# Kernel optimization log

Measured on AMD Instinct MI355X. Metric: run time of the kernel, lower is better.

Reference implementation:

```python
import jax, jax.numpy as jnp
import numpy as np

N_NODES = 100000
N_EDGES = 1600000
F_IN = 128      # dataset.num_features
HID = 128       # hidden_dim (heads=1)
HID_POST = 128  # hidden_dim_post
EDGE_DIM = 16
N_CLASSES = 16
NEG_SLOPE = 0.2  # PyG GATConv default leaky_relu slope


def setup_inputs() -> dict:
    key = jax.random.key(0)
    ks = jax.random.split(key, 16)
    s = 0.1  # weight scale
    inp = {
        "x": jax.random.normal(ks[0], (N_NODES, F_IN), jnp.float32),
        "edge_attr": jax.random.normal(ks[1], (N_EDGES, EDGE_DIM), jnp.float32),
        "W0": jax.random.normal(ks[2], (F_IN, HID), jnp.float32) * s,
        "a_src0": jax.random.normal(ks[3], (HID,), jnp.float32) * s,
        "a_dst0": jax.random.normal(ks[4], (HID,), jnp.float32) * s,
        "We0": jax.random.normal(ks[5], (EDGE_DIM, HID), jnp.float32) * s,
        "a_e0": jax.random.normal(ks[6], (HID,), jnp.float32) * s,
        "b0": jnp.zeros((HID,), jnp.float32),
        "W1": jax.random.normal(ks[7], (HID, HID), jnp.float32) * s,
        "a_src1": jax.random.normal(ks[8], (HID,), jnp.float32) * s,
        "a_dst1": jax.random.normal(ks[9], (HID,), jnp.float32) * s,
        "We1": jax.random.normal(ks[10], (EDGE_DIM, HID), jnp.float32) * s,
        "a_e1": jax.random.normal(ks[11], (HID,), jnp.float32) * s,
        "b1": jnp.zeros((HID,), jnp.float32),
        "lin1_w": jax.random.normal(ks[12], (HID, HID_POST), jnp.float32) * s,
        "lin1_b": jnp.zeros((HID_POST,), jnp.float32),
        "lin2_w": jax.random.normal(ks[13], (HID_POST, N_CLASSES), jnp.float32) * s,
        "lin2_b": jnp.zeros((N_CLASSES,), jnp.float32),
        "edge_index": jax.random.randint(ks[14], (2, N_EDGES), 0, N_NODES, jnp.int64),
    }
    return inp


def gat_conv(x, src, dst, edge_attr, W, a_s, a_d, We, a_e, b):
    """PyG GATConv, heads=1, edge_dim set, add_self_loops=True (fill_value='mean')."""
    n = x.shape[0]
    xl = x @ W                       # [N, HID] shared lin for src/dst
    alpha_src_n = xl @ a_s           # [N]
    alpha_dst_n = xl @ a_d           # [N]
    # self loops: edge_attr filled with per-target-node mean of incoming edge_attr
    deg = jax.ops.segment_sum(jnp.ones(src.shape[0], x.dtype), dst, num_segments=n)
    ea_mean = jax.ops.segment_sum(edge_attr, dst, num_segments=n) / jnp.maximum(deg, 1.0)[:, None]
    loop = jnp.arange(n, dtype=src.dtype)
    src_f = jnp.concatenate([src, loop])
    dst_f = jnp.concatenate([dst, loop])
    ea_f = jnp.concatenate([edge_attr, ea_mean], axis=0)  # [E+N, EDGE_DIM]
    alpha_edge = (ea_f @ We) @ a_e                        # [E+N]
    alpha = jax.nn.leaky_relu(
        alpha_src_n[src_f] + alpha_dst_n[dst_f] + alpha_edge, NEG_SLOPE
    )
    # segment softmax over destination node (every node has its self loop -> nonempty)
    amax = jax.ops.segment_max(alpha, dst_f, num_segments=n)
    ex = jnp.exp(alpha - amax[dst_f])
    denom = jax.ops.segment_sum(ex, dst_f, num_segments=n)
    w = ex / denom[dst_f]                                 # [E+N]
    out = jax.ops.segment_sum(xl[src_f] * w[:, None], dst_f, num_segments=n)
    return out + b


def reference(x, edge_attr, W0, a_src0, a_dst0, We0, a_e0, b0,
              W1, a_src1, a_dst1, We1, a_e1, b1,
              lin1_w, lin1_b, lin2_w, lin2_b, edge_index):
    src, dst = edge_index[0], edge_index[1]
    # dropout layers are identity in eval mode
    h = jax.nn.relu(gat_conv(x, src, dst, edge_attr, W0, a_src0, a_dst0, We0, a_e0, b0))
    h = jax.nn.relu(gat_conv(h, src, dst, edge_attr, W1, a_src1, a_dst1, We1, a_e1, b1))
    h = jax.nn.relu(h @ lin1_w + lin1_b)
    logits = h @ lin2_w + lin2_b
    return jax.nn.log_softmax(logits, axis=-1)
```

## Files before the change

### kernel.cpp

```cpp
#include <hip/hip_runtime.h>
#include <math.h>

#define N_NODES 100000
#define N_EDGES 1600000
#define NEG 0.2f
#define MAXDEG 128
#define WPB 4
#define NBK 391
#define CHK 6250

__device__ __forceinline__ float lrelu(float x){ return x > 0.f ? x : NEG*x; }
__device__ __forceinline__ unsigned short f2bf(float f){
  unsigned int u = __float_as_uint(f);
  u += 0x7FFFu + ((u >> 16) & 1u);
  return (unsigned short)(u >> 16);
}


__global__ __launch_bounds__(512) void k_count(const int* __restrict__ dst, int* __restrict__ gcount){
  __shared__ unsigned hist[NBK];
  int t = threadIdx.x;
  for (int b=t; b<NBK; b+=512) hist[b]=0;
  __syncthreads();
  int base = blockIdx.x * CHK;
  for (int i=t; i<CHK; i+=512){
    int d = dst[base+i];
    atomicAdd(&hist[d>>8], 1u);
  }
  __syncthreads();
  for (int b=t; b<NBK; b+=512){
    unsigned h = hist[b];
    if (h) atomicAdd(&gcount[b], (int)h);
  }
}

__global__ __launch_bounds__(512) void k_bscan(const int* __restrict__ gcount,
    int* __restrict__ gbase, int* __restrict__ gcursor,
    const float* __restrict__ We0, const float* __restrict__ ae0,
    const float* __restrict__ We1, const float* __restrict__ ae1,
    float* __restrict__ wea01, int* __restrict__ rowptr){
  __shared__ int s[512];
  int t = threadIdx.x;
  int v = (t<NBK)? gcount[t] : 0;
  s[t]=v; __syncthreads();
  for (int off=1; off<512; off<<=1){
    int u = (t>=off)? s[t-off]:0; __syncthreads();
    s[t]+=u; __syncthreads();
  }
  if (t<NBK){ int e = s[t]-v; gbase[t]=e; gcursor[t]=e; }
  if (t==NBK) gbase[NBK]=N_EDGES;
  if (t==0) rowptr[N_NODES]=N_EDGES;
  if (t<32){
    const float* W = (t<16)? We0 : We1;
    const float* a = (t<16)? ae0 : ae1;
    int r = t & 15;
    float acc = 0.f;
    #pragma unroll
    for (int j=0;j<128;j++) acc += W[r*128+j]*a[j];
    wea01[t]=acc;
  }
}

__global__ __launch_bounds__(512) void k_part(const int* __restrict__ dst,
    int* __restrict__ gcursor, unsigned* __restrict__ part){
  __shared__ unsigned hist[NBK];
  __shared__ int bbase[NBK];
  __shared__ unsigned cur[NBK];
  int t = threadIdx.x;
  for (int b=t; b<NBK; b+=512) hist[b]=0;
  __syncthreads();
  int base = blockIdx.x * CHK;
  for (int i=t; i<CHK; i+=512) atomicAdd(&hist[dst[base+i]>>8], 1u);
  __syncthreads();
  for (int b=t; b<NBK; b+=512){
    unsigned h = hist[b];
    bbase[b] = h ? atomicAdd(&gcursor[b], (int)h) : 0;
    cur[b]=0;
  }
  __syncthreads();
  for (int i=t; i<CHK; i+=512){
    int e = base+i;
    int d = dst[e];
    int bin = d>>8;
    unsigned off = atomicAdd(&cur[bin], 1u);
    part[bbase[bin]+(int)off] = (unsigned)e | ((unsigned)(d&255)<<21);
  }
}

__global__ __launch_bounds__(512) void k_build(const int* __restrict__ gbase,
    const unsigned* __restrict__ part, const int* __restrict__ src,
    const float* __restrict__ eatt, const float* __restrict__ wea01,
    int* __restrict__ rowptr, uint4* __restrict__ csr){
  __shared__ unsigned cnt[256];
  __shared__ int rb[256];
  __shared__ unsigned s[256];
  __shared__ float wea[32];
  int t = threadIdx.x;
  int b = blockIdx.x;
  int lo = gbase[b], hi = gbase[b+1];
  if (t<32) wea[t]=wea01[t];
  if (t<256) cnt[t]=0;
  __syncthreads();
  for (int i=lo+t; i<hi; i+=512) atomicAdd(&cnt[part[i]>>21], 1u);
  __syncthreads();
  if (t<256) s[t]=cnt[t];
  __syncthreads();
  for (int off=1; off<256; off<<=1){
    unsigned u = 0;
    if (t<256 && t>=off) u = s[t-off];
    __syncthreads();
    if (t<256) s[t]+=u;
    __syncthreads();
  }
  if (t<256){
    int bn = lo + (int)(s[t]-cnt[t]);
    rb[t]=bn;
    int node = (b<<8)+t;
    if (node < N_NODES) rowptr[node]=bn;
    cnt[t]=0;
  }
  __syncthreads();
  for (int i=lo+t; i<hi; i+=512){
    unsigned p = part[i];
    int eid = (int)(p & 0x1FFFFFu);
    int dl  = (int)(p >> 21);
    const float4* pe = (const float4*)(eatt + (size_t)eid*16);
    float4 a0=pe[0], a1=pe[1], a2=pe[2], a3=pe[3];
    float f0 = a0.x*wea[0] +a0.y*wea[1] +a0.z*wea[2] +a0.w*wea[3]
             + a1.x*wea[4] +a1.y*wea[5] +a1.z*wea[6] +a1.w*wea[7]
             + a2.x*wea[8] +a2.y*wea[9] +a2.z*wea[10]+a2.w*wea[11]
             + a3.x*wea[12]+a3.y*wea[13]+a3.z*wea[14]+a3.w*wea[15];
    float f1 = a0.x*wea[16]+a0.y*wea[17]+a0.z*wea[18]+a0.w*wea[19]
             + a1.x*wea[20]+a1.y*wea[21]+a1.z*wea[22]+a1.w*wea[23]
             + a2.x*wea[24]+a2.y*wea[25]+a2.z*wea[26]+a2.w*wea[27]
             + a3.x*wea[28]+a3.y*wea[29]+a3.z*wea[30]+a3.w*wea[31];
    int sx = src[eid];
    unsigned off = atomicAdd(&cnt[dl], 1u);
    csr[rb[dl]+(int)off] = make_uint4((unsigned)sx, __float_as_uint(f0), __float_as_uint(f1), 0u);
  }
}

__global__ __launch_bounds__(256) void k_gemm(const float* __restrict__ X, const float* __restrict__ W,
    const float* __restrict__ bias, float* __restrict__ Y, unsigned short* __restrict__ Ybf,
    const float* __restrict__ a_s, const float* __restrict__ a_d,
    float* __restrict__ asrc, float* __restrict__ adst, int M, int relu){
  __shared__ float Xs[16][68];
  __shared__ float Ws[16][128];
  __shared__ float as_s[128], ad_s[128];
  int t = threadIdx.x;
  if (a_s && t < 128){ as_s[t] = a_s[t]; ad_s[t] = a_d[t]; }
  int row0 = blockIdx.x * 64;
  int tc = t & 15, tr = t >> 4;
  int c0 = tc*8, r0 = tr*4;
  int lr = t >> 2, lc = (t & 3) << 2;
  int wk = t >> 4, wc = (t & 15) * 8;
  float acc[4][8];
  #pragma unroll
  for (int i=0;i<4;i++)
    #pragma unroll
    for (int j=0;j<8;j++) acc[i][j]=0.f;
  int gr = row0 + lr;
  for (int k0=0; k0<128; k0+=16){
    float4 xv = make_float4(0.f,0.f,0.f,0.f);
    if (gr < M) xv = *(const float4*)(X + (size_t)gr*128 + k0 + lc);
    float4 wv0 = *(const float4*)(W + (size_t)(k0+wk)*128 + wc);
    float4 wv1 = *(const float4*)(W + (size_t)(k0+wk)*128 + wc + 4);
    __syncthreads();
    Xs[lc+0][lr]=xv.x; Xs[lc+1][lr]=xv.y; Xs[lc+2][lr]=xv.z; Xs[lc+3][lr]=xv.w;
    *(float4*)&Ws[wk][wc]   = wv0;
    *(float4*)&Ws[wk][wc+4] = wv1;
    __syncthreads();
    #pragma unroll
    for (int kk=0;kk<16;kk++){
      float4 a  = *(const float4*)&Xs[kk][r0];
      float4 b0 = *(const float4*)&Ws[kk][c0];
      float4 b1 = *(const float4*)&Ws[kk][c0+4];
      float av[4] = {a.x,a.y,a.z,a.w};
      float bv[8] = {b0.x,b0.y,b0.z,b0.w,b1.x,b1.y,b1.z,b1.w};
      #pragma unroll
      for (int i=0;i<4;i++)
        #pragma unroll
        for (int j=0;j<8;j++) acc[i][j] += av[i]*bv[j];
    }
  }
  #pragma unroll
  for (int i=0;i<4;i++){
    int r = row0 + r0 + i;
    float v[8];
    #pragma unroll
    for (int j=0;j<8;j++){
      float u = acc[i][j] + (bias ? bias[c0+j] : 0.f);
      v[j] = relu ? fmaxf(u, 0.f) : u;
    }
    if (r < M){
      if (Y){
        *(float4*)(Y + (size_t)r*128 + c0)     = make_float4(v[0],v[1],v[2],v[3]);
        *(float4*)(Y + (size_t)r*128 + c0 + 4) = make_float4(v[4],v[5],v[6],v[7]);
      }
      if (Ybf){
        uint4 pk;
        pk.x = (unsigned)f2bf(v[0]) | ((unsigned)f2bf(v[1])<<16);
        pk.y = (unsigned)f2bf(v[2]) | ((unsigned)f2bf(v[3])<<16);
        pk.z = (unsigned)f2bf(v[4]) | ((unsigned)f2bf(v[5])<<16);
        pk.w = (unsigned)f2bf(v[6]) | ((unsigned)f2bf(v[7])<<16);
        *(uint4*)(Ybf + (size_t)r*128 + c0) = pk;
      }
    }
    if (a_s){
      float s=0.f, d=0.f;
      #pragma unroll
      for (int j=0;j<8;j++){ s += v[j]*as_s[c0+j]; d += v[j]*ad_s[c0+j]; }
      #pragma unroll
      for (int off=1; off<16; off<<=1){ s += __shfl_xor(s,off); d += __shfl_xor(d,off); }
      if ((t & 15)==0 && r < M){ asrc[r]=s; adst[r]=d; }
    }
  }
}

__global__ __launch_bounds__(256) void k_agg(const int* __restrict__ rowptr, const uint4* __restrict__ csr,
    const float* __restrict__ asrc, const float* __restrict__ adst,
    const unsigned short* __restrict__ xlbf,
    const float* __restrict__ bias, float* __restrict__ out, int relu, int layer){
  int w = threadIdx.x >> 6;
  int lane = threadIdx.x & 63;
  int n = blockIdx.x * WPB + w;
  __shared__ float2 eb[WPB][MAXDEG];
  const char* xbase = (const char*)xlbf;
  int s0 = rowptr[n], s1 = rowptr[n+1];
  int deg = s1 - s0;
  float adst_n = adst[n];
  float m_edge = -1e30f;
  float sae = 0.f;
  for (int base=0; base<deg; base+=64){
    int i = base + lane;
    float a = -1e30f;
    if (i < deg){
      uint4 p4 = csr[s0 + i];
      int sx = (int)p4.x;
      float ae = __uint_as_float(layer ? p4.z : p4.y);
      float av = lrelu(asrc[sx] + adst_n + ae);
      if (i < MAXDEG) eb[w][i] = make_float2(av, __uint_as_float((unsigned)sx << 8));
      a = av;
      sae += ae;
    }
    for (int off=32; off; off>>=1) a = fmaxf(a, __shfl_xor(a, off));
    m_edge = fmaxf(m_edge, a);
  }
  for (int off=32; off; off>>=1) sae += __shfl_xor(sae, off);
  float aloop_n = sae / fmaxf((float)deg, 1.f);
  float al = lrelu(asrc[n] + adst_n + aloop_n);
  float m = fmaxf(m_edge, al);
  float p = 0.f;
  for (int i=lane; i<deg; i+=64){
    float av;
    if (i < MAXDEG) av = eb[w][i].x;
    else { uint4 p4 = csr[s0+i];
           av = lrelu(asrc[p4.x] + adst_n + __uint_as_float(layer ? p4.z : p4.y)); }
    float ev = __expf(av - m);
    if (i < MAXDEG) eb[w][i].x = ev;
    p += ev;
  }
  for (int off=32; off; off>>=1) p += __shfl_xor(p, off);
  float wl = __expf(al - m);
  float denom = p + wl;
  __syncthreads();
  int g = lane >> 4, cl = lane & 15;
  unsigned clb = (unsigned)(cl << 4);
  float acc[8];
  #pragma unroll
  for (int j=0;j<8;j++) acc[j]=0.f;
  if (g == 0){
    uint4 v = *(const uint4*)(xbase + (((unsigned)n << 8) + clb));
    unsigned int uu[4] = {v.x,v.y,v.z,v.w};
    #pragma unroll
    for (int q=0;q<4;q++){
      acc[2*q]   += wl * __uint_as_float(uu[q] << 16);
      acc[2*q+1] += wl * __uint_as_float(uu[q] & 0xFFFF0000u);
    }
  }
  if (deg <= MAXDEG){
    int dfull = deg & ~7;
    for (int i=0; i<dfull; i+=8){
      float2 e0 = eb[w][i+g];
      float2 e1 = eb[w][i+4+g];
      uint4 v0 = *(const uint4*)(xbase + (__float_as_uint(e0.y) + clb));
      uint4 v1 = *(const uint4*)(xbase + (__float_as_uint(e1.y) + clb));
      unsigned int uu0[4] = {v0.x,v0.y,v0.z,v0.w};
      unsigned int uu1[4] = {v1.x,v1.y,v1.z,v1.w};
      #pragma unroll
      for (int q=0;q<4;q++){
        acc[2*q]   += e0.x * __uint_as_float(uu0[q] << 16);
        acc[2*q+1] += e0.x * __uint_as_float(uu0[q] & 0xFFFF0000u);
      }
      #pragma unroll
      for (int q=0;q<4;q++){
        acc[2*q]   += e1.x * __uint_as_float(uu1[q] << 16);
        acc[2*q+1] += e1.x * __uint_as_float(uu1[q] & 0xFFFF0000u);
      }
    }
    for (int i=dfull; i<deg; i+=4){
      int idx = i + g;
      float we = 0.f; unsigned off = (unsigned)n << 8;
      if (idx < deg){ float2 e = eb[w][idx]; we = e.x; off = __float_as_uint(e.y); }
      uint4 v = *(const uint4*)(xbase + (off + clb));
      unsigned int uu[4] = {v.x,v.y,v.z,v.w};
      #pragma unroll
      for (int q=0;q<4;q++){
        acc[2*q]   += we * __uint_as_float(uu[q] << 16);
        acc[2*q+1] += we * __uint_as_float(uu[q] & 0xFFFF0000u);
      }
    }
  } else {
    for (int i=0; i<deg; i+=8){
      int idx0 = i + g, idx1 = i + 4 + g;
      int sx0 = n, sx1 = n; float we0 = 0.f, we1 = 0.f;
      if (idx0 < deg){
        if (idx0 < MAXDEG){ float2 e = eb[w][idx0]; we0 = e.x; sx0 = (int)(__float_as_uint(e.y) >> 8); }
        else { uint4 p4 = csr[s0+idx0]; sx0 = (int)p4.x;
               we0 = __expf(lrelu(asrc[sx0] + adst_n + __uint_as_float(layer ? p4.z : p4.y)) - m); }
      }
      if (idx1 < deg){
        if (idx1 < MAXDEG){ float2 e = eb[w][idx1]; we1 = e.x; sx1 = (int)(__float_as_uint(e.y) >> 8); }
        else { uint4 p4 = csr[s0+idx1]; sx1 = (int)p4.x;
               we1 = __expf(lrelu(asrc[sx1] + adst_n + __uint_as_float(layer ? p4.z : p4.y)) - m); }
      }
      uint4 v0 = *(const uint4*)(xbase + (((unsigned)sx0 << 8) + clb));
      uint4 v1 = *(const uint4*)(xbase + (((unsigned)sx1 << 8) + clb));
      unsigned int uu0[4] = {v0.x,v0.y,v0.z,v0.w};
      unsigned int uu1[4] = {v1.x,v1.y,v1.z,v1.w};
      #pragma unroll
      for (int q=0;q<4;q++){
        acc[2*q]   += we0 * __uint_as_float(uu0[q] << 16);
        acc[2*q+1] += we0 * __uint_as_float(uu0[q] & 0xFFFF0000u);
      }
      #pragma unroll
      for (int q=0;q<4;q++){
        acc[2*q]   += we1 * __uint_as_float(uu1[q] << 16);
        acc[2*q+1] += we1 * __uint_as_float(uu1[q] & 0xFFFF0000u);
      }
    }
  }
  #pragma unroll
  for (int j=0;j<8;j++){
    acc[j] += __shfl_xor(acc[j], 16);
    acc[j] += __shfl_xor(acc[j], 32);
  }
  if (lane < 16){
    float inv = 1.f/denom;
    float4 b0 = *(const float4*)(bias + cl*8);
    float4 b1 = *(const float4*)(bias + cl*8 + 4);
    float o[8];
    o[0]=acc[0]*inv+b0.x; o[1]=acc[1]*inv+b0.y; o[2]=acc[2]*inv+b0.z; o[3]=acc[3]*inv+b0.w;
    o[4]=acc[4]*inv+b1.x; o[5]=acc[5]*inv+b1.y; o[6]=acc[6]*inv+b1.z; o[7]=acc[7]*inv+b1.w;
    if (relu){
      #pragma unroll
      for (int j=0;j<8;j++) o[j]=fmaxf(o[j],0.f);
    }
    *(float4*)(out + (size_t)n*128 + cl*8)     = make_float4(o[0],o[1],o[2],o[3]);
    *(float4*)(out + (size_t)n*128 + cl*8 + 4) = make_float4(o[4],o[5],o[6],o[7]);
  }
}

__global__ __launch_bounds__(256) void k_mlp(const float* __restrict__ X, const float* __restrict__ W,
    const float* __restrict__ bias, const float* __restrict__ w2, const float* __restrict__ b2,
    float* __restrict__ out, int M){
  __shared__ float Xs[16][68];
  __shared__ float Ws[16][128];
  __shared__ float b2s[16];
  int t = threadIdx.x;
  int row0 = blockIdx.x * 64;
  int tc = t & 15, tr = t >> 4;
  int c0 = tc*8, r0 = tr*4;
  int lr = t >> 2, lc = (t & 3) << 2;
  int wk = t >> 4, wc = (t & 15) * 8;
  float acc[4][8];
  #pragma unroll
  for (int i=0;i<4;i++)
    #pragma unroll
    for (int j=0;j<8;j++) acc[i][j]=0.f;
  int gr = row0 + lr;
  for (int k0=0; k0<128; k0+=16){
    float4 xv = make_float4(0.f,0.f,0.f,0.f);
    if (gr < M) xv = *(const float4*)(X + (size_t)gr*128 + k0 + lc);
    float4 wv0 = *(const float4*)(W + (size_t)(k0+wk)*128 + wc);
    float4 wv1 = *(const float4*)(W + (size_t)(k0+wk)*128 + wc + 4);
    __syncthreads();
    Xs[lc+0][lr]=xv.x; Xs[lc+1][lr]=xv.y; Xs[lc+2][lr]=xv.z; Xs[lc+3][lr]=xv.w;
    *(float4*)&Ws[wk][wc]   = wv0;
    *(float4*)&Ws[wk][wc+4] = wv1;
    __syncthreads();
    #pragma unroll
    for (int kk=0;kk<16;kk++){
      float4 a  = *(const float4*)&Xs[kk][r0];
      float4 b0 = *(const float4*)&Ws[kk][c0];
      float4 b1 = *(const float4*)&Ws[kk][c0+4];
      float av[4] = {a.x,a.y,a.z,a.w};
      float bv[8] = {b0.x,b0.y,b0.z,b0.w,b1.x,b1.y,b1.z,b1.w};
      #pragma unroll
      for (int i=0;i<4;i++)
        #pragma unroll
        for (int j=0;j<8;j++) acc[i][j] += av[i]*bv[j];
    }
  }
  __syncthreads();
  float* wflat = &Ws[0][0];
  #pragma unroll
  for (int i=0;i<2;i++) ((float4*)wflat)[t + i*256] = ((const float4*)w2)[t + i*256];
  if (t < 16) b2s[t] = b2[t];
  float4 bba = *(const float4*)(bias + c0);
  float4 bbb = *(const float4*)(bias + c0 + 4);
  float bb[8] = {bba.x,bba.y,bba.z,bba.w,bbb.x,bbb.y,bbb.z,bbb.w};
  #pragma unroll
  for (int i=0;i<4;i++)
    #pragma unroll
    for (int j=0;j<8;j++) acc[i][j] = fmaxf(acc[i][j] + bb[j], 0.f);
  __syncthreads();
  float A0=0.f, A1=0.f, A2=0.f, A3=0.f;
  int sl = (tc+1) & 15;
  #pragma unroll 4
  for (int s=0; s<16; s++){
    int cls = (tc + s) & 15;
    const float* wp = wflat + (size_t)c0*16 + cls;
    float p0=0.f,p1=0.f,p2=0.f,p3=0.f;
    #pragma unroll
    for (int j=0;j<8;j++){
      float wv = wp[j*16];
      p0 += acc[0][j]*wv; p1 += acc[1][j]*wv; p2 += acc[2][j]*wv; p3 += acc[3][j]*wv;
    }
    A0+=p0; A1+=p1; A2+=p2; A3+=p3;
    A0=__shfl(A0,sl,16); A1=__shfl(A1,sl,16); A2=__shfl(A2,sl,16); A3=__shfl(A3,sl,16);
  }
  float A[4] = {A0,A1,A2,A3};
  float bcls = b2s[tc];
  #pragma unroll
  for (int i=0;i<4;i++){
    float v = A[i] + bcls;
    float m = v;
    #pragma unroll
    for (int off=1; off<16; off<<=1) m = fmaxf(m, __shfl_xor(m, off, 16));
    float ex = __expf(v - m);
    float sum = ex;
    #pragma unroll
    for (int off=1; off<16; off<<=1) sum += __shfl_xor(sum, off, 16);
    float lse = m + __logf(sum);
    int r = row0 + r0 + i;
    if (r < M) out[(size_t)r*16 + tc] = v - lse;
  }
}

extern "C" void kernel_launch(void* const* d_in, const int* in_sizes, int n_in,
                              void* d_out, int out_size, void* d_ws, size_t ws_size,
                              hipStream_t stream){
  const float* x    = (const float*)d_in[0];
  const float* eatt = (const float*)d_in[1];
  const float* W0   = (const float*)d_in[2];
  const float* as0  = (const float*)d_in[3];
  const float* ad0  = (const float*)d_in[4];
  const float* We0  = (const float*)d_in[5];
  const float* ae0  = (const float*)d_in[6];
  const float* b0   = (const float*)d_in[7];
  const float* W1   = (const float*)d_in[8];
  const float* as1  = (const float*)d_in[9];
  const float* ad1  = (const float*)d_in[10];
  const float* We1  = (const float*)d_in[11];
  const float* ae1  = (const float*)d_in[12];
  const float* b1   = (const float*)d_in[13];
  const float* l1w  = (const float*)d_in[14];
  const float* l1b  = (const float*)d_in[15];
  const float* l2w  = (const float*)d_in[16];
  const float* l2b  = (const float*)d_in[17];
  const int*   ei   = (const int*)d_in[18];
  const int* srcI = ei;
  const int* dstI = ei + N_EDGES;
  float* out = (float*)d_out;

  char* p = (char*)d_ws;
  auto alloc = [&](size_t bytes)->char*{ char* r = p; p += (bytes + 255) & ~255ull; return r; };
  unsigned short* Abf = (unsigned short*)alloc((size_t)N_NODES*128*2);
  float* B       = (float*)alloc((size_t)N_NODES*128*4);
  float* asrc    = (float*)alloc((size_t)N_NODES*4);
  float* adst    = (float*)alloc((size_t)N_NODES*4);
  int* rowptr  = (int*)alloc((size_t)(N_NODES+1)*4);
  uint4* csr   = (uint4*)alloc((size_t)N_EDGES*16);
  int* gcount  = (int*)alloc(400*4);
  int* gbase   = (int*)alloc(400*4);
  int* gcursor = (int*)alloc(400*4);
  float* wea01 = (float*)alloc(128);
  unsigned* part = (unsigned*)B;

  const int NB_W = N_NODES/WPB;
  const int NB_G = (N_NODES+63)/64;

  hipMemsetAsync(gcount, 0, 400*4, stream);
  k_count<<<256,512,0,stream>>>(dstI, gcount);
  k_bscan<<<1,  512,0,stream>>>(gcount, gbase, gcursor, We0, ae0, We1, ae1, wea01, rowptr);
  k_part <<<256,512,0,stream>>>(dstI, gcursor, part);
  k_gemm <<<NB_G,256,0,stream>>>(x, W0, nullptr, nullptr, Abf, as0, ad0, asrc, adst, N_NODES, 0);
  k_build<<<NBK,512,0,stream>>>(gbase, part, srcI, eatt, wea01, rowptr, csr);

  k_agg  <<<NB_W,256,0,stream>>>(rowptr, csr, asrc, adst, Abf, b0, B, 1, 0);

  k_gemm <<<NB_G,256,0,stream>>>(B, W1, nullptr, nullptr, Abf, as1, ad1, asrc, adst, N_NODES, 0);
  k_agg  <<<NB_W,256,0,stream>>>(rowptr, csr, asrc, adst, Abf, b1, B, 1, 1);

  k_mlp  <<<NB_G,256,0,stream>>>(B, l1w, l1b, l2w, l2b, out, N_NODES);
}
```

Measured before the change: 634.4 us.

## Precompute edge attention terms coalesced and split CSR fill into quarter blocks

Edge-attribute attention scalars are now computed in the counting pass by reading edge_attr sequentially, and stored as a compact float2 per edge. This replaces the random 64-byte gathers the build step used to do. The CSR build is split into a per-bin counting kernel that records per-quarter prefix offsets and a fill kernel launched with four times as many blocks, each handling a quarter of a bin. The aim is more parallelism and fewer scattered reads, at the cost of an extra kernel launch and an extra pass over the partition array.

```diff
diff --git a/kernel.cpp b/kernel.cpp
--- a/kernel.cpp
+++ b/kernel.cpp
@@ -17,115 +17,31 @@
 }
 
 
-__global__ __launch_bounds__(512) void k_count(const int* __restrict__ dst, int* __restrict__ gcount){
-  __shared__ unsigned hist[NBK];
-  int t = threadIdx.x;
-  for (int b=t; b<NBK; b+=512) hist[b]=0;
-  __syncthreads();
-  int base = blockIdx.x * CHK;
-  for (int i=t; i<CHK; i+=512){
-    int d = dst[base+i];
-    atomicAdd(&hist[d>>8], 1u);
-  }
-  __syncthreads();
-  for (int b=t; b<NBK; b+=512){
-    unsigned h = hist[b];
-    if (h) atomicAdd(&gcount[b], (int)h);
-  }
-}
-
-__global__ __launch_bounds__(512) void k_bscan(const int* __restrict__ gcount,
-    int* __restrict__ gbase, int* __restrict__ gcursor,
+__global__ __launch_bounds__(512) void k_count(const int* __restrict__ dst, const float* __restrict__ eatt,
     const float* __restrict__ We0, const float* __restrict__ ae0,
     const float* __restrict__ We1, const float* __restrict__ ae1,
-    float* __restrict__ wea01, int* __restrict__ rowptr){
-  __shared__ int s[512];
-  int t = threadIdx.x;
-  int v = (t<NBK)? gcount[t] : 0;
-  s[t]=v; __syncthreads();
-  for (int off=1; off<512; off<<=1){
-    int u = (t>=off)? s[t-off]:0; __syncthreads();
-    s[t]+=u; __syncthreads();
-  }
-  if (t<NBK){ int e = s[t]-v; gbase[t]=e; gcursor[t]=e; }
-  if (t==NBK) gbase[NBK]=N_EDGES;
-  if (t==0) rowptr[N_NODES]=N_EDGES;
-  if (t<32){
-    const float* W = (t<16)? We0 : We1;
-    const float* a = (t<16)? ae0 : ae1;
+    int* __restrict__ gcount, float2* __restrict__ ae01){
+  __shared__ unsigned hist[NBK];
+  __shared__ float wea[32];
+  int t = threadIdx.x;
+  if (t < 32){
+    const float* W = (t < 16) ? We0 : We1;
+    const float* a = (t < 16) ? ae0 : ae1;
     int r = t & 15;
     float acc = 0.f;
     #pragma unroll
     for (int j=0;j<128;j++) acc += W[r*128+j]*a[j];
-    wea01[t]=acc;
-  }
-}
-
-__global__ __launch_bounds__(512) void k_part(const int* __restrict__ dst,
-    int* __restrict__ gcursor, unsigned* __restrict__ part){
-  __shared__ unsigned hist[NBK];
-  __shared__ int bbase[NBK];
-  __shared__ unsigned cur[NBK];
-  int t = threadIdx.x;
+    wea[t] = acc;
+  }
   for (int b=t; b<NBK; b+=512) hist[b]=0;
   __syncthreads();
   int base = blockIdx.x * CHK;
-  for (int i=t; i<CHK; i+=512) atomicAdd(&hist[dst[base+i]>>8], 1u);
-  __syncthreads();
-  for (int b=t; b<NBK; b+=512){
-    unsigned h = hist[b];
-    bbase[b] = h ? atomicAdd(&gcursor[b], (int)h) : 0;
-    cur[b]=0;
-  }
-  __syncthreads();
   for (int i=t; i<CHK; i+=512){
     int e = base+i;
     int d = dst[e];
-    int bin = d>>8;
-    unsigned off = atomicAdd(&cur[bin], 1u);
-    part[bbase[bin]+(int)off] = (unsigned)e | ((unsigned)(d&255)<<21);
-  }
-}
-
-__global__ __launch_bounds__(512) void k_build(const int* __restrict__ gbase,
-    const unsigned* __restrict__ part, const int* __restrict__ src,
-    const float* __restrict__ eatt, const float* __restrict__ wea01,
-    int* __restrict__ rowptr, uint4* __restrict__ csr){
-  __shared__ unsigned cnt[256];
-  __shared__ int rb[256];
-  __shared__ unsigned s[256];
-  __shared__ float wea[32];
-  int t = threadIdx.x;
-  int b = blockIdx.x;
-  int lo = gbase[b], hi = gbase[b+1];
-  if (t<32) wea[t]=wea01[t];
-  if (t<256) cnt[t]=0;
-  __syncthreads();
-  for (int i=lo+t; i<hi; i+=512) atomicAdd(&cnt[part[i]>>21], 1u);
-  __syncthreads();
-  if (t<256) s[t]=cnt[t];
-  __syncthreads();
-  for (int off=1; off<256; off<<=1){
-    unsigned u = 0;
-    if (t<256 && t>=off) u = s[t-off];
-    __syncthreads();
-    if (t<256) s[t]+=u;
-    __syncthreads();
-  }
-  if (t<256){
-    int bn = lo + (int)(s[t]-cnt[t]);
-    rb[t]=bn;
-    int node = (b<<8)+t;
-    if (node < N_NODES) rowptr[node]=bn;
-    cnt[t]=0;
-  }
-  __syncthreads();
-  for (int i=lo+t; i<hi; i+=512){
-    unsigned p = part[i];
-    int eid = (int)(p & 0x1FFFFFu);
-    int dl  = (int)(p >> 21);
-    const float4* pe = (const float4*)(eatt + (size_t)eid*16);
-    float4 a0=pe[0], a1=pe[1], a2=pe[2], a3=pe[3];
+    atomicAdd(&hist[d>>8], 1u);
+    const float4* p = (const float4*)(eatt + (size_t)e*16);
+    float4 a0=p[0], a1=p[1], a2=p[2], a3=p[3];
     float f0 = a0.x*wea[0] +a0.y*wea[1] +a0.z*wea[2] +a0.w*wea[3]
              + a1.x*wea[4] +a1.y*wea[5] +a1.z*wea[6] +a1.w*wea[7]
              + a2.x*wea[8] +a2.y*wea[9] +a2.z*wea[10]+a2.w*wea[11]
@@ -134,9 +50,127 @@
              + a1.x*wea[20]+a1.y*wea[21]+a1.z*wea[22]+a1.w*wea[23]
              + a2.x*wea[24]+a2.y*wea[25]+a2.z*wea[26]+a2.w*wea[27]
              + a3.x*wea[28]+a3.y*wea[29]+a3.z*wea[30]+a3.w*wea[31];
-    int sx = src[eid];
-    unsigned off = atomicAdd(&cnt[dl], 1u);
-    csr[rb[dl]+(int)off] = make_uint4((unsigned)sx, __float_as_uint(f0), __float_as_uint(f1), 0u);
+    ae01[e] = make_float2(f0, f1);
+  }
+  __syncthreads();
+  for (int b=t; b<NBK; b+=512){
+    unsigned h = hist[b];
+    if (h) atomicAdd(&gcount[b], (int)h);
+  }
+}
+
+__global__ __launch_bounds__(512) void k_bscan(const int* __restrict__ gcount,
+    int* __restrict__ gbase, int* __restrict__ gcursor, int* __restrict__ rowptr){
+  __shared__ int s[512];
+  int t = threadIdx.x;
+  int v = (t<NBK)? gcount[t] : 0;
+  s[t]=v; __syncthreads();
+  for (int off=1; off<512; off<<=1){
+    int u = (t>=off)? s[t-off]:0; __syncthreads();
+    s[t]+=u; __syncthreads();
+  }
+  if (t<NBK){ int e = s[t]-v; gbase[t]=e; gcursor[t]=e; }
+  if (t==NBK) gbase[NBK]=N_EDGES;
+  if (t==0) rowptr[N_NODES]=N_EDGES;
+}
+
+__global__ __launch_bounds__(512) void k_part(const int* __restrict__ dst,
+    int* __restrict__ gcursor, unsigned* __restrict__ part){
+  __shared__ unsigned hist[NBK];
+  __shared__ int bbase[NBK];
+  __shared__ unsigned cur[NBK];
+  int t = threadIdx.x;
+  for (int b=t; b<NBK; b+=512) hist[b]=0;
+  __syncthreads();
+  int base = blockIdx.x * CHK;
+  for (int i=t; i<CHK; i+=512) atomicAdd(&hist[dst[base+i]>>8], 1u);
+  __syncthreads();
+  for (int b=t; b<NBK; b+=512){
+    unsigned h = hist[b];
+    bbase[b] = h ? atomicAdd(&gcursor[b], (int)h) : 0;
+    cur[b]=0;
+  }
+  __syncthreads();
+  for (int i=t; i<CHK; i+=512){
+    int e = base+i;
+    int d = dst[e];
+    int bin = d>>8;
+    unsigned off = atomicAdd(&cur[bin], 1u);
+    part[bbase[bin]+(int)off] = (unsigned)e | ((unsigned)(d&255)<<21);
+  }
+}
+
+__global__ __launch_bounds__(512) void k_build_a(const int* __restrict__ gbase,
+    const unsigned* __restrict__ part, int* __restrict__ rowptr, int* __restrict__ qpre){
+  __shared__ unsigned cntq[4][256];
+  __shared__ unsigned s[256];
+  int t = threadIdx.x;
+  int b = blockIdx.x;
+  int lo = gbase[b], hi = gbase[b+1];
+  int len = hi - lo;
+  int q1 = lo + ((len*1)>>2), q2 = lo + ((len*2)>>2), q3 = lo + ((len*3)>>2);
+  for (int k=t; k<1024; k+=512) ((unsigned*)cntq)[k] = 0u;
+  __syncthreads();
+  for (int i=lo+t; i<hi; i+=512){
+    unsigned p = part[i];
+    int node = (int)(p >> 21);
+    int q = (i>=q1) + (i>=q2) + (i>=q3);
+    atomicAdd(&cntq[q][node], 1u);
+  }
+  __syncthreads();
+  unsigned tot = 0;
+  if (t<256){ tot = cntq[0][t]+cntq[1][t]+cntq[2][t]+cntq[3][t]; s[t]=tot; }
+  __syncthreads();
+  for (int off=1; off<256; off<<=1){
+    unsigned u = 0;
+    if (t<256 && t>=off) u = s[t-off];
+    __syncthreads();
+    if (t<256) s[t]+=u;
+    __syncthreads();
+  }
+  if (t<256){
+    int rb = lo + (int)(s[t]-tot);
+    int node = (b<<8)+t;
+    if (node < N_NODES) rowptr[node]=rb;
+    int run = rb;
+    #pragma unroll
+    for (int q=0;q<4;q++){
+      qpre[((b*4+q)<<8) + t] = run;
+      run += (int)cntq[q][t];
+    }
+  }
+}
+
+__global__ __launch_bounds__(256) void k_fill(const int* __restrict__ gbase,
+    const unsigned* __restrict__ part, const int* __restrict__ src,
+    const float2* __restrict__ ae01, const int* __restrict__ qpre,
+    uint4* __restrict__ csr){
+  __shared__ unsigned cur[256];
+  int t = threadIdx.x;
+  int bq = blockIdx.x;
+  int b = bq >> 2, q = bq & 3;
+  int lo = gbase[b], hi = gbase[b+1];
+  int len = hi - lo;
+  int ql = lo + ((len*q)>>2);
+  int qh = lo + ((len*(q+1))>>2);
+  cur[t] = (unsigned)qpre[(bq<<8) + t];
+  __syncthreads();
+  for (int i = ql + t; i < qh; i += 512){
+    int i1 = i + 256;
+    bool has1 = i1 < qh;
+    unsigned p0 = part[i];
+    unsigned p1 = has1 ? part[i1] : p0;
+    int e0 = (int)(p0 & 0x1FFFFFu), n0 = (int)(p0 >> 21);
+    int e1 = (int)(p1 & 0x1FFFFFu), n1 = (int)(p1 >> 21);
+    float2 ae_a = ae01[e0];
+    float2 ae_b = ae01[e1];
+    int s0 = src[e0], s1 = src[e1];
+    unsigned o0 = atomicAdd(&cur[n0], 1u);
+    csr[o0] = make_uint4((unsigned)s0, __float_as_uint(ae_a.x), __float_as_uint(ae_a.y), 0u);
+    if (has1){
+      unsigned o1 = atomicAdd(&cur[n1], 1u);
+      csr[o1] = make_uint4((unsigned)s1, __float_as_uint(ae_b.x), __float_as_uint(ae_b.y), 0u);
+    }
   }
 }
 
@@ -485,18 +519,21 @@
   int* gcount  = (int*)alloc(400*4);
   int* gbase   = (int*)alloc(400*4);
   int* gcursor = (int*)alloc(400*4);
-  float* wea01 = (float*)alloc(128);
-  unsigned* part = (unsigned*)B;
+  char* Bc = (char*)B;
+  unsigned* part = (unsigned*)Bc;
+  int*      qpre = (int*)(Bc + 6400000);
+  float2*   ae01 = (float2*)(Bc + 6400000 + 1602560);
 
   const int NB_W = N_NODES/WPB;
   const int NB_G = (N_NODES+63)/64;
 
   hipMemsetAsync(gcount, 0, 400*4, stream);
-  k_count<<<256,512,0,stream>>>(dstI, gcount);
-  k_bscan<<<1,  512,0,stream>>>(gcount, gbase, gcursor, We0, ae0, We1, ae1, wea01, rowptr);
+  k_count<<<256,512,0,stream>>>(dstI, eatt, We0, ae0, We1, ae1, gcount, ae01);
+  k_bscan<<<1,  512,0,stream>>>(gcount, gbase, gcursor, rowptr);
   k_part <<<256,512,0,stream>>>(dstI, gcursor, part);
+  k_build_a<<<NBK,512,0,stream>>>(gbase, part, rowptr, qpre);
   k_gemm <<<NB_G,256,0,stream>>>(x, W0, nullptr, nullptr, Abf, as0, ad0, asrc, adst, N_NODES, 0);
-  k_build<<<NBK,512,0,stream>>>(gbase, part, srcI, eatt, wea01, rowptr, csr);
+  k_fill <<<NBK*4,256,0,stream>>>(gbase, part, srcI, ae01, qpre, csr);
 
   k_agg  <<<NB_W,256,0,stream>>>(rowptr, csr, asrc, adst, Abf, b0, B, 1, 0);
 
```

New measurement: 611.6 us. 3.6% less time.
